# Kernel optimization log

Measured on AMD Instinct MI355X. Metric: run time of the kernel, lower is better.

Reference implementation:

```python
import jax, jax.numpy as jnp
import numpy as np
from jax import lax

D_MODEL = 1024
EXPAND = 2
D_INNER = EXPAND * D_MODEL  # 2048
D_STATE = 16
D_CONV = 4
DT_RANK = -(-D_INNER // 16)  # ceil(d_inner/16) = 128
BATCH, SEQLEN = 2, 1024
LN_EPS = 1e-5


def setup_inputs() -> dict:
    key = jax.random.key(0)
    ks = jax.random.split(key, 8)
    s = lambda n: 1.0 / np.sqrt(n)
    x = jax.random.normal(ks[0], (BATCH, SEQLEN, D_MODEL), jnp.float32)
    ln_gamma = jnp.ones((D_MODEL,), jnp.float32)
    ln_beta = jnp.zeros((D_MODEL,), jnp.float32)
    in_proj_w = jax.random.normal(ks[1], (D_MODEL, 2 * D_INNER), jnp.float32) * s(D_MODEL)
    conv_w = jax.random.normal(ks[2], (D_INNER, D_CONV), jnp.float32) * s(D_CONV)
    conv_b = jnp.zeros((D_INNER,), jnp.float32)
    x_proj_w = jax.random.normal(ks[3], (D_INNER, DT_RANK + 2 * D_STATE), jnp.float32) * s(D_INNER)
    dt_proj_w = jax.random.uniform(ks[4], (DT_RANK, D_INNER), jnp.float32,
                                   -DT_RANK ** -0.5, DT_RANK ** -0.5)
    # dt bias init: inverse-softplus of dt ~ LogUniform(1e-3, 1e-1)
    dt = jnp.exp(jax.random.uniform(ks[5], (D_INNER,), jnp.float32)
                 * (np.log(0.1) - np.log(0.001)) + np.log(0.001))
    dt = jnp.clip(dt, 1e-4)
    dt_proj_b = dt + jnp.log(-jnp.expm1(-dt))
    A_log = jnp.log(jnp.tile(jnp.arange(1, D_STATE + 1, dtype=jnp.float32)[None, :],
                             (D_INNER, 1)))  # (D_INNER, D_STATE)
    D_param = jnp.ones((D_INNER,), jnp.float32)
    out_proj_w = jax.random.normal(ks[6], (D_INNER, D_MODEL), jnp.float32) * s(D_INNER)
    return {"x": x, "ln_gamma": ln_gamma, "ln_beta": ln_beta, "in_proj_w": in_proj_w,
            "conv_w": conv_w, "conv_b": conv_b, "x_proj_w": x_proj_w,
            "dt_proj_w": dt_proj_w, "dt_proj_b": dt_proj_b, "A_log": A_log,
            "D_param": D_param, "out_proj_w": out_proj_w}


def _layernorm(x, gamma, beta):
    mu = jnp.mean(x, -1, keepdims=True)
    var = jnp.mean(jnp.square(x - mu), -1, keepdims=True)
    return (x - mu) * lax.rsqrt(var + LN_EPS) * gamma + beta


def reference(x, ln_gamma, ln_beta, in_proj_w, conv_w, conv_b, x_proj_w,
              dt_proj_w, dt_proj_b, A_log, D_param, out_proj_w):
    B, L, _ = x.shape
    residual = x
    h = _layernorm(x, ln_gamma, ln_beta)
    xz = h @ in_proj_w                               # (B, L, 2*Di)
    xb, z = jnp.split(xz, 2, axis=-1)                # each (B, L, Di)

    # Depthwise causal conv1d (left pad d_conv-1, truncate to L)
    xp = jnp.pad(xb, ((0, 0), (D_CONV - 1, 0), (0, 0)))
    xc = sum(xp[:, k:k + L, :] * conv_w[:, k] for k in range(D_CONV)) + conv_b
    xb = jax.nn.silu(xc)                             # (B, L, Di)

    # Selective SSM
    xpj = xb @ x_proj_w                              # (B, L, dt_rank + 2N)
    dt_r = xpj[..., :DT_RANK]
    B_mat = xpj[..., DT_RANK:DT_RANK + D_STATE]      # (B, L, N)
    C_mat = xpj[..., DT_RANK + D_STATE:]             # (B, L, N)
    delta = jax.nn.softplus(dt_r @ dt_proj_w + dt_proj_b)  # (B, L, Di)
    A = -jnp.exp(A_log)                              # (Di, N)
    dA = jnp.exp(delta[..., None] * A)               # (B, L, Di, N)
    dBx = delta[..., None] * B_mat[:, :, None, :] * xb[..., None]  # (B, L, Di, N)

    def step(hcar, inp):
        dA_t, dBx_t, C_t = inp                       # (B,Di,N),(B,Di,N),(B,N)
        hcar = dA_t * hcar + dBx_t
        y_t = jnp.einsum('bdn,bn->bd', hcar, C_t)
        return hcar, y_t

    h0 = jnp.zeros((B, D_INNER, D_STATE), xb.dtype)
    _, ys = lax.scan(step, h0, (dA.transpose(1, 0, 2, 3),
                                dBx.transpose(1, 0, 2, 3),
                                C_mat.transpose(1, 0, 2)))
    y = ys.transpose(1, 0, 2) + xb * D_param         # (B, L, Di)

    y = y * jax.nn.silu(z)
    return y @ out_proj_w + residual
```

## Files before the change

kernel.cpp:

```cpp
#include <hip/hip_runtime.h>
#include <hip/hip_bf16.h>

#define D_MODEL 1024
#define D_INNER 2048
#define NPROJ   4096
#define D_STATE 16
#define DT_RANK 128
#define XPJ_N   160
#define SEQLEN  1024
#define BATCH   2
#define NTOK    2048
#define CHUNK   32
#define NCHUNK  (SEQLEN / CHUNK)
#define LOG2_NCHUNK 5
#define SPLITK  8
#define OP_SPLITK 4

typedef short short8 __attribute__((ext_vector_type(8)));
typedef float f32x4 __attribute__((ext_vector_type(4)));

__device__ __forceinline__ float sigmoidf_(float x) { return 1.f / (1.f + __expf(-x)); }
__device__ __forceinline__ ushort f2bf_bits(float f) {
    __hip_bfloat16 h = __float2bfloat16(f);
    return *(ushort*)&h;
}
__device__ __forceinline__ float bf2f(ushort u) {
    union { unsigned int i; float f; } v;
    v.i = ((unsigned int)u) << 16;
    return v.f;
}

__global__ __launch_bounds__(256) void ln_kernel(const float* __restrict__ x,
                                                 const float* __restrict__ g,
                                                 const float* __restrict__ be,
                                                 ushort* __restrict__ hb)
{
    int row = blockIdx.x;
    const float4* xr = (const float4*)(x + (long)row * D_MODEL);
    float4 v = xr[threadIdx.x];
    float s1 = v.x + v.y + v.z + v.w;
    float s2 = v.x*v.x + v.y*v.y + v.z*v.z + v.w*v.w;
    for (int off = 32; off >= 1; off >>= 1) {
        s1 += __shfl_down(s1, off);
        s2 += __shfl_down(s2, off);
    }
    __shared__ float red[8];
    int wid = threadIdx.x >> 6;
    if ((threadIdx.x & 63) == 0) { red[wid] = s1; red[4 + wid] = s2; }
    __syncthreads();
    float mu  = (red[0] + red[1] + red[2] + red[3]) * (1.f / D_MODEL);
    float ex2 = (red[4] + red[5] + red[6] + red[7]) * (1.f / D_MODEL);
    float inv = rsqrtf(ex2 - mu * mu + 1e-5f);
    float4 g4 = ((const float4*)g)[threadIdx.x];
    float4 b4 = ((const float4*)be)[threadIdx.x];
    ushort4 o;
    o.x = f2bf_bits((v.x - mu) * inv * g4.x + b4.x);
    o.y = f2bf_bits((v.y - mu) * inv * g4.y + b4.y);
    o.z = f2bf_bits((v.z - mu) * inv * g4.z + b4.z);
    o.w = f2bf_bits((v.w - mu) * inv * g4.w + b4.w);
    *(ushort4*)(hb + (long)row * D_MODEL + threadIdx.x * 4) = o;
}

__global__ __launch_bounds__(256) void transpose_bf16_kernel(const float* __restrict__ in,
                                                             ushort* __restrict__ out,
                                                             int R, int C)
{
    __shared__ float tile[64][65];
    int c0 = blockIdx.x * 64, r0 = blockIdx.y * 64;
    #pragma unroll
    for (int i = 0; i < 16; ++i) {
        int idx = threadIdx.x + i * 256;
        int r = idx >> 6, c = idx & 63;
        tile[r][c] = (r0 + r < R && c0 + c < C) ? in[(long)(r0 + r) * C + (c0 + c)] : 0.f;
    }
    __syncthreads();
    #pragma unroll
    for (int i = 0; i < 16; ++i) {
        int idx = threadIdx.x + i * 256;
        int cc = idx >> 6, rr = idx & 63;
        if (c0 + cc < C && r0 + rr < R)
            out[(long)(c0 + cc) * R + (r0 + rr)] = f2bf_bits(tile[rr][cc]);
    }
}

template <int EPI, int OBF>
__global__ __launch_bounds__(256) void gemm_mfma_kernel(const ushort* __restrict__ A,
                                                        const ushort* __restrict__ Bt,
                                                        const float* __restrict__ bias,
                                                        const float* __restrict__ resid,
                                                        float* __restrict__ Cf,
                                                        ushort* __restrict__ Cb,
                                                        int M, int N, int K, int lda, int ldb)
{
    long zoff = (long)blockIdx.z;
    A  += zoff * K;
    Bt += zoff * K;
    if (OBF == 0) Cf += zoff * (long)M * N;
    __shared__ __align__(16) ushort Al[128 * 32];
    __shared__ __align__(16) ushort Bl[128 * 32];
    int tid = threadIdx.x;
    int lane = tid & 63;
    int w = tid >> 6, wr = w >> 1, wc = w & 1;
    int m0 = blockIdx.y * 128, n0 = blockIdx.x * 128;
    f32x4 acc[4][4];
    #pragma unroll
    for (int m = 0; m < 4; ++m)
        #pragma unroll
        for (int n = 0; n < 4; ++n) acc[m][n] = (f32x4){0.f, 0.f, 0.f, 0.f};
    int l15 = lane & 15, kq = lane >> 4;

    for (int k0 = 0; k0 < K; k0 += 32) {
        #pragma unroll
        for (int i = 0; i < 2; ++i) {
            int s = i * 256 + tid;
            int row = s >> 2, kg = s & 3;
            int kgl = kg ^ ((row >> 1) & 3);
            __builtin_amdgcn_global_load_lds(
                (const __attribute__((address_space(1))) void*)(A + (long)(m0 + row) * lda + k0 + kgl * 8),
                (__attribute__((address_space(3))) void*)(Al + s * 8), 16, 0, 0);
            __builtin_amdgcn_global_load_lds(
                (const __attribute__((address_space(1))) void*)(Bt + (long)(n0 + row) * ldb + k0 + kgl * 8),
                (__attribute__((address_space(3))) void*)(Bl + s * 8), 16, 0, 0);
        }
        __syncthreads();
        short8 af[4], bf[4];
        #pragma unroll
        for (int m = 0; m < 4; ++m) {
            int row = wr * 64 + m * 16 + l15;
            af[m] = *(const short8*)&Al[row * 32 + (kq ^ ((row >> 1) & 3)) * 8];
        }
        #pragma unroll
        for (int n = 0; n < 4; ++n) {
            int row = wc * 64 + n * 16 + l15;
            bf[n] = *(const short8*)&Bl[row * 32 + (kq ^ ((row >> 1) & 3)) * 8];
        }
        #pragma unroll
        for (int m = 0; m < 4; ++m)
            #pragma unroll
            for (int n = 0; n < 4; ++n)
                acc[m][n] = __builtin_amdgcn_mfma_f32_16x16x32_bf16(af[m], bf[n], acc[m][n], 0, 0, 0);
        __syncthreads();
    }
    #pragma unroll
    for (int m = 0; m < 4; ++m) {
        #pragma unroll
        for (int n = 0; n < 4; ++n) {
            #pragma unroll
            for (int r = 0; r < 4; ++r) {
                int row = m0 + wr * 64 + m * 16 + kq * 4 + r;
                int col = n0 + wc * 64 + n * 16 + l15;
                float v = acc[m][n][r];
                if (EPI == 1) {
                    v += bias[col];
                    v = (v > 20.f) ? v : log1pf(__expf(v));
                } else if (EPI == 2) {
                    v += resid[(long)row * N + col];
                }
                if (OBF) Cb[(long)row * N + col] = f2bf_bits(v);
                else     Cf[(long)row * N + col] = v;
            }
        }
    }
}

template <int EPI, int OBF>
__global__ __launch_bounds__(256) void gemm_mfma64_kernel(const ushort* __restrict__ A,
                                                          const ushort* __restrict__ Bt,
                                                          const float* __restrict__ bias,
                                                          const float* __restrict__ resid,
                                                          float* __restrict__ Cf,
                                                          ushort* __restrict__ Cb,
                                                          int M, int N, int K)
{
    __shared__ __align__(16) ushort Al[128 * 32];
    __shared__ __align__(16) ushort Bl[64 * 32];
    int tid = threadIdx.x;
    int lane = tid & 63;
    int w = tid >> 6, wr = w >> 1, wc = w & 1;
    int m0 = blockIdx.y * 128, n0 = blockIdx.x * 64;
    f32x4 acc[4][2];
    #pragma unroll
    for (int m = 0; m < 4; ++m)
        #pragma unroll
        for (int n = 0; n < 2; ++n) acc[m][n] = (f32x4){0.f, 0.f, 0.f, 0.f};
    int l15 = lane & 15, kq = lane >> 4;

    for (int k0 = 0; k0 < K; k0 += 32) {
        #pragma unroll
        for (int i = 0; i < 2; ++i) {
            int s = i * 256 + tid;
            int row = s >> 2, kg = s & 3;
            int kgl = kg ^ ((row >> 1) & 3);
            __builtin_amdgcn_global_load_lds(
                (const __attribute__((address_space(1))) void*)(A + (long)(m0 + row) * K + k0 + kgl * 8),
                (__attribute__((address_space(3))) void*)(Al + s * 8), 16, 0, 0);
        }
        {
            int s = tid;
            int row = s >> 2, kg = s & 3;
            int kgl = kg ^ ((row >> 1) & 3);
            __builtin_amdgcn_global_load_lds(
                (const __attribute__((address_space(1))) void*)(Bt + (long)(n0 + row) * K + k0 + kgl * 8),
                (__attribute__((address_space(3))) void*)(Bl + s * 8), 16, 0, 0);
        }
        __syncthreads();
        short8 af[4], bf[2];
        #pragma unroll
        for (int m = 0; m < 4; ++m) {
            int row = wr * 64 + m * 16 + l15;
            af[m] = *(const short8*)&Al[row * 32 + (kq ^ ((row >> 1) & 3)) * 8];
        }
        #pragma unroll
        for (int n = 0; n < 2; ++n) {
            int row = wc * 32 + n * 16 + l15;
            bf[n] = *(const short8*)&Bl[row * 32 + (kq ^ ((row >> 1) & 3)) * 8];
        }
        #pragma unroll
        for (int m = 0; m < 4; ++m)
            #pragma unroll
            for (int n = 0; n < 2; ++n)
                acc[m][n] = __builtin_amdgcn_mfma_f32_16x16x32_bf16(af[m], bf[n], acc[m][n], 0, 0, 0);
        __syncthreads();
    }
    #pragma unroll
    for (int m = 0; m < 4; ++m) {
        #pragma unroll
        for (int n = 0; n < 2; ++n) {
            #pragma unroll
            for (int r = 0; r < 4; ++r) {
                int row = m0 + wr * 64 + m * 16 + kq * 4 + r;
                int col = n0 + wc * 32 + n * 16 + l15;
                float v = acc[m][n][r];
                if (EPI == 1) {
                    v += bias[col];
                    v = (v > 20.f) ? v : log1pf(__expf(v));
                } else if (EPI == 2) {
                    v += resid[(long)row * N + col];
                }
                if (OBF) Cb[(long)row * N + col] = f2bf_bits(v);
                else     Cf[(long)row * N + col] = v;
            }
        }
    }
}

__global__ __launch_bounds__(256) void reduce_out_kernel(const float* __restrict__ Ppart,
                                                         const float* __restrict__ resid,
                                                         float* __restrict__ out)
{
    long i = (long)blockIdx.x * 256 + threadIdx.x;
    const long STRIDE = (long)NTOK * D_MODEL / 4;
    float4 s = ((const float4*)Ppart)[i];
    #pragma unroll
    for (int k = 1; k < OP_SPLITK; ++k) {
        float4 p = ((const float4*)Ppart)[k * STRIDE + i];
        s.x += p.x; s.y += p.y; s.z += p.z; s.w += p.w;
    }
    float4 r = ((const float4*)resid)[i];
    s.x += r.x; s.y += r.y; s.z += r.z; s.w += r.w;
    ((float4*)out)[i] = s;
}

__global__ __launch_bounds__(256) void gemm4_mfma_kernel(const ushort* __restrict__ A,
                                                         const ushort* __restrict__ Bt,
                                                         float* __restrict__ Ppart,
                                                         int M, int K)
{
    __shared__ __align__(16) ushort Al[64 * 32];
    __shared__ __align__(16) ushort Bl[160 * 32];
    int tid = threadIdx.x;
    int lane = tid & 63;
    int w = tid >> 6, wr = w >> 1, wc = w & 1;
    int sk = blockIdx.x;
    int m0 = blockIdx.y * 64;
    int kbase = sk * (K / SPLITK);
    f32x4 acc[2][5];
    #pragma unroll
    for (int m = 0; m < 2; ++m)
        #pragma unroll
        for (int n = 0; n < 5; ++n) acc[m][n] = (f32x4){0.f, 0.f, 0.f, 0.f};
    int l15 = lane & 15, kq = lane >> 4;

    for (int ks = 0; ks < K / SPLITK; ks += 32) {
        int k0 = kbase + ks;
        {
            int s = tid;
            int row = s >> 2, kg = s & 3;
            int kgl = kg ^ ((row >> 1) & 3);
            __builtin_amdgcn_global_load_lds(
                (const __attribute__((address_space(1))) void*)(A + (long)(m0 + row) * K + k0 + kgl * 8),
                (__attribute__((address_space(3))) void*)(Al + s * 8), 16, 0, 0);
        }
        #pragma unroll
        for (int i = 0; i < 3; ++i) {
            int s = i * 256 + tid;
            if (s < 640) {
                int row = s >> 2, kg = s & 3;
                int kgl = kg ^ ((row >> 1) & 3);
                __builtin_amdgcn_global_load_lds(
                    (const __attribute__((address_space(1))) void*)(Bt + (long)row * K + k0 + kgl * 8),
                    (__attribute__((address_space(3))) void*)(Bl + s * 8), 16, 0, 0);
            }
        }
        __syncthreads();
        short8 af[2], bf[5];
        #pragma unroll
        for (int m = 0; m < 2; ++m) {
            int row = wr * 32 + m * 16 + l15;
            af[m] = *(const short8*)&Al[row * 32 + (kq ^ ((row >> 1) & 3)) * 8];
        }
        #pragma unroll
        for (int n = 0; n < 5; ++n) {
            int row = wc * 80 + n * 16 + l15;
            bf[n] = *(const short8*)&Bl[row * 32 + (kq ^ ((row >> 1) & 3)) * 8];
        }
        #pragma unroll
        for (int m = 0; m < 2; ++m)
            #pragma unroll
            for (int n = 0; n < 5; ++n)
                acc[m][n] = __builtin_amdgcn_mfma_f32_16x16x32_bf16(af[m], bf[n], acc[m][n], 0, 0, 0);
        __syncthreads();
    }
    float* P = Ppart + (long)sk * M * XPJ_N;
    #pragma unroll
    for (int m = 0; m < 2; ++m) {
        #pragma unroll
        for (int n = 0; n < 5; ++n) {
            #pragma unroll
            for (int r = 0; r < 4; ++r) {
                int row = m0 + wr * 32 + m * 16 + kq * 4 + r;
                int col = wc * 80 + n * 16 + l15;
                P[(long)row * XPJ_N + col] = acc[m][n][r];
            }
        }
    }
}

__global__ __launch_bounds__(256) void reduce_xpj_kernel(const float* __restrict__ Ppart,
                                                         float* __restrict__ xpj,
                                                         ushort* __restrict__ dtr)
{
    long i = (long)blockIdx.x * 256 + threadIdx.x;
    float s = 0.f;
    #pragma unroll
    for (int k = 0; k < SPLITK; ++k) s += Ppart[k * (long)NTOK * XPJ_N + i];
    xpj[i] = s;
    int col = (int)(i % XPJ_N);
    long row = i / XPJ_N;
    if (col < DT_RANK) dtr[row * DT_RANK + col] = f2bf_bits(s);
}

__global__ __launch_bounds__(256) void conv_silu_kernel(const ushort* __restrict__ xzb,
                                                        const float* __restrict__ cw,
                                                        const float* __restrict__ cb,
                                                        ushort* __restrict__ xbb)
{
    long i = (long)blockIdx.x * 256 + threadIdx.x;
    int d = (int)(i & (D_INNER - 1));
    long tok = i >> 11;
    int l = (int)(tok & (SEQLEN - 1));
    float w0 = cw[d * 4 + 0], w1 = cw[d * 4 + 1], w2 = cw[d * 4 + 2], w3 = cw[d * 4 + 3];
    float acc = cb[d];
    acc += bf2f(xzb[tok * NPROJ + d]) * w3;
    if (l >= 1) acc += bf2f(xzb[(tok - 1) * NPROJ + d]) * w2;
    if (l >= 2) acc += bf2f(xzb[(tok - 2) * NPROJ + d]) * w1;
    if (l >= 3) acc += bf2f(xzb[(tok - 3) * NPROJ + d]) * w0;
    float v = acc * sigmoidf_(acc);
    xbb[i] = f2bf_bits(v);
}

__global__ __launch_bounds__(256) void scan_partial_kernel(const ushort* __restrict__ deltab,
                                                           const ushort* __restrict__ xbb,
                                                           const float* __restrict__ xpj,
                                                           const float* __restrict__ A_log,
                                                           float* __restrict__ Pout,
                                                           float* __restrict__ Hout)
{
    int tid = threadIdx.x;
    int j = tid & 3, grp = tid >> 2;
    long gidx = (long)blockIdx.x * 64 + grp;
    int d = (int)(gidx & (D_INNER - 1));
    int c = (int)((gidx >> 11) & (NCHUNK - 1));
    int b = (int)(gidx >> (11 + LOG2_NCHUNK));
    float4 al = *(const float4*)&A_log[d * D_STATE + 4 * j];
    float a0 = -__expf(al.x), a1 = -__expf(al.y), a2 = -__expf(al.z), a3 = -__expf(al.w);
    float h0 = 0.f, h1 = 0.f, h2 = 0.f, h3 = 0.f, cum = 0.f;
    long tok0 = (long)b * SEQLEN + c * CHUNK;
    const ushort* dp = deltab + tok0 * D_INNER + d;
    const ushort* xp = xbb + tok0 * D_INNER + d;
    const float* Bp = xpj + tok0 * XPJ_N + DT_RANK + 4 * j;
    for (int t = 0; t < CHUNK; ++t) {
        float dl = bf2f(*dp);
        float x  = bf2f(*xp);
        float4 Bv = *(const float4*)Bp;
        dp += D_INNER; xp += D_INNER; Bp += XPJ_N;
        cum += dl;
        float ux = dl * x;
        h0 = __expf(dl * a0) * h0 + ux * Bv.x;
        h1 = __expf(dl * a1) * h1 + ux * Bv.y;
        h2 = __expf(dl * a2) * h2 + ux * Bv.z;
        h3 = __expf(dl * a3) * h3 + ux * Bv.w;
    }
    long o = gidx * D_STATE + 4 * j;
    *(float4*)&Pout[o] = (float4){__expf(a0 * cum), __expf(a1 * cum), __expf(a2 * cum), __expf(a3 * cum)};
    *(float4*)&Hout[o] = (float4){h0, h1, h2, h3};
}

__global__ __launch_bounds__(256) void scan_chunkscan_kernel(const float* __restrict__ P,
                                                             const float* __restrict__ H,
                                                             float* __restrict__ hinit)
{
    long i = (long)blockIdx.x * 256 + threadIdx.x;
    int n = (int)(i & (D_STATE - 1));
    int d = (int)((i >> 4) & (D_INNER - 1));
    int b = (int)(i >> 15);
    float h = 0.f;
    for (int c = 0; c < NCHUNK; ++c) {
        long o = ((((long)b * NCHUNK + c) * D_INNER + d) * D_STATE) + n;
        hinit[o] = h;
        h = P[o] * h + H[o];
    }
}

__global__ __launch_bounds__(256) void scan_final_kernel(const ushort* __restrict__ deltab,
                                                         const ushort* __restrict__ xbb,
                                                         const float* __restrict__ xpj,
                                                         const ushort* __restrict__ xzb,
                                                         const float* __restrict__ A_log,
                                                         const float* __restrict__ Dp,
                                                         const float* __restrict__ hinit,
                                                         ushort* __restrict__ yb)
{
    int tid = threadIdx.x;
    int j = tid & 3, grp = tid >> 2;
    long gidx = (long)blockIdx.x * 64 + grp;
    int d = (int)(gidx & (D_INNER - 1));
    int c = (int)((gidx >> 11) & (NCHUNK - 1));
    int b = (int)(gidx >> (11 + LOG2_NCHUNK));
    float4 al = *(const float4*)&A_log[d * D_STATE + 4 * j];
    float a0 = -__expf(al.x), a1 = -__expf(al.y), a2 = -__expf(al.z), a3 = -__expf(al.w);
    float dpar = Dp[d];
    float4 hv = *(const float4*)&hinit[gidx * D_STATE + 4 * j];
    float h0 = hv.x, h1 = hv.y, h2 = hv.z, h3 = hv.w;
    long tok0 = (long)b * SEQLEN + c * CHUNK;
    const ushort* dp = deltab + tok0 * D_INNER + d;
    const ushort* xp = xbb + tok0 * D_INNER + d;
    const float* Bp = xpj + tok0 * XPJ_N + DT_RANK + 4 * j;
    const float* Cp = Bp + D_STATE;
    const ushort* zp = xzb + tok0 * NPROJ + D_INNER + d;
    ushort* yp = yb + tok0 * D_INNER + d;
    for (int t = 0; t < CHUNK; ++t) {
        float dl = bf2f(*dp);
        float x  = bf2f(*xp);
        float4 Bv = *(const float4*)Bp;
        float4 Cv = *(const float4*)Cp;
        dp += D_INNER; xp += D_INNER; Bp += XPJ_N; Cp += XPJ_N;
        float ux = dl * x;
        h0 = __expf(dl * a0) * h0 + ux * Bv.x;
        h1 = __expf(dl * a1) * h1 + ux * Bv.y;
        h2 = __expf(dl * a2) * h2 + ux * Bv.z;
        h3 = __expf(dl * a3) * h3 + ux * Bv.w;
        float p = h0 * Cv.x + h1 * Cv.y + h2 * Cv.z + h3 * Cv.w;
        p += __shfl_xor(p, 1);
        p += __shfl_xor(p, 2);
        if (j == 0) {
            float z = bf2f(*zp);
            float y = p + x * dpar;
            *yp = f2bf_bits(y * (z * sigmoidf_(z)));
        }
        zp += NPROJ; yp += D_INNER;
    }
}

extern "C" void kernel_launch(void* const* d_in, const int* in_sizes, int n_in,
                              void* d_out, int out_size, void* d_ws, size_t ws_size,
                              hipStream_t stream) {
    const float* x         = (const float*)d_in[0];
    const float* ln_gamma  = (const float*)d_in[1];
    const float* ln_beta   = (const float*)d_in[2];
    const float* in_proj_w = (const float*)d_in[3];
    const float* conv_w    = (const float*)d_in[4];
    const float* conv_b    = (const float*)d_in[5];
    const float* x_proj_w  = (const float*)d_in[6];
    const float* dt_proj_w = (const float*)d_in[7];
    const float* dt_proj_b = (const float*)d_in[8];
    const float* A_log     = (const float*)d_in[9];
    const float* D_param   = (const float*)d_in[10];
    const float* out_proj_w= (const float*)d_in[11];
    float* out = (float*)d_out;

    float* ws = (float*)d_ws;
    float* h     = ws;
    float* xz    = h     + (long)NTOK * D_MODEL;
    float* xb    = xz    + (long)NTOK * NPROJ;
    float* xpj   = xb    + (long)NTOK * D_INNER;
    float* delta = xpj   + (long)NTOK * XPJ_N;
    float* yfin  = delta + (long)NTOK * D_INNER;

    const long PH = (long)BATCH * NCHUNK * D_INNER * D_STATE;
    ushort* h_bf16   = (ushort*)h;
    ushort* DTT      = (ushort*)(h + 1048576);
    float*  hinit    = h;
    ushort* xz_bf16  = (ushort*)xz;
    ushort* W7T      = (ushort*)(xz + 4194304);
    ushort* W2T      = (ushort*)xb;
    ushort* xb_bf16  = (ushort*)xb;
    ushort* XPT      = (ushort*)xpj;
    ushort* delta_bf16 = (ushort*)delta;
    float*  Ppart    = yfin;
    ushort* dtr      = (ushort*)(yfin + (long)SPLITK * NTOK * XPJ_N);
    float*  Pbuf     = yfin;
    float*  Hbuf     = yfin + PH;
    ushort* y_bf16   = (ushort*)yfin;
    float*  PpartO   = xb;

    transpose_bf16_kernel<<<dim3(NPROJ / 64, D_MODEL / 64), 256, 0, stream>>>(
        in_proj_w, W2T, D_MODEL, NPROJ);
    transpose_bf16_kernel<<<dim3(D_MODEL / 64, D_INNER / 64), 256, 0, stream>>>(
        out_proj_w, W7T, D_INNER, D_MODEL);

    ln_kernel<<<NTOK, 256, 0, stream>>>(x, ln_gamma, ln_beta, h_bf16);

    gemm_mfma_kernel<0, 1><<<dim3(NPROJ / 128, NTOK / 128), 256, 0, stream>>>(
        h_bf16, W2T, nullptr, nullptr, nullptr, xz_bf16,
        NTOK, NPROJ, D_MODEL, D_MODEL, D_MODEL);

    conv_silu_kernel<<<(NTOK * D_INNER) / 256, 256, 0, stream>>>(
        xz_bf16, conv_w, conv_b, xb_bf16);

    transpose_bf16_kernel<<<dim3((XPJ_N + 63) / 64, D_INNER / 64), 256, 0, stream>>>(
        x_proj_w, XPT, D_INNER, XPJ_N);
    transpose_bf16_kernel<<<dim3(D_INNER / 64, DT_RANK / 64), 256, 0, stream>>>(
        dt_proj_w, DTT, DT_RANK, D_INNER);

    gemm4_mfma_kernel<<<dim3(SPLITK, NTOK / 64), 256, 0, stream>>>(
        xb_bf16, XPT, Ppart, NTOK, D_INNER);
    reduce_xpj_kernel<<<(NTOK * XPJ_N) / 256, 256, 0, stream>>>(Ppart, xpj, dtr);

    gemm_mfma64_kernel<1, 1><<<dim3(D_INNER / 64, NTOK / 128), 256, 0, stream>>>(
        dtr, DTT, dt_proj_b, nullptr, nullptr, delta_bf16, NTOK, D_INNER, DT_RANK);

    scan_partial_kernel<<<(BATCH * NCHUNK * D_INNER) / 64, 256, 0, stream>>>(
        delta_bf16, xb_bf16, xpj, A_log, Pbuf, Hbuf);
    scan_chunkscan_kernel<<<(BATCH * D_INNER * D_STATE) / 256, 256, 0, stream>>>(
        Pbuf, Hbuf, hinit);
    scan_final_kernel<<<(BATCH * NCHUNK * D_INNER) / 64, 256, 0, stream>>>(
        delta_bf16, xb_bf16, xpj, xz_bf16, A_log, D_param, hinit, y_bf16);

    gemm_mfma_kernel<0, 0><<<dim3(D_MODEL / 128, NTOK / 128, OP_SPLITK), 256, 0, stream>>>(
        y_bf16, W7T, nullptr, nullptr, PpartO, nullptr, NTOK, D_MODEL, D_INNER / OP_SPLITK,
        D_INNER, D_INNER);
    reduce_out_kernel<<<(NTOK * D_MODEL / 4) / 256, 256, 0, stream>>>(PpartO, x, out);
}
```

Before: 203.9 us.

## Store scan inputs channel-major so scan kernels read contiguous vectors

The in_proj GEMM epilogue now writes x to a compact buffer and z transposed (channel-major), and the dt_proj GEMM writes delta transposed. A new bf16 transpose kernel produces a channel-major copy of xb. The scan kernels read 8 timesteps per vector load instead of strided scalar loads, and use exp2f with pre-scaled A. The scan output is produced channel-major and transposed back before the out_proj GEMM. This replaces strided per-timestep global accesses in the scans, at the cost of two extra transpose launches and a larger workspace layout.

```diff
diff --git a/kernel.cpp b/kernel.cpp
--- a/kernel.cpp
+++ b/kernel.cpp
@@ -12,11 +12,12 @@
 #define NTOK    2048
 #define CHUNK   32
 #define NCHUNK  (SEQLEN / CHUNK)
-#define LOG2_NCHUNK 5
 #define SPLITK  8
 #define OP_SPLITK 4
 
 typedef short short8 __attribute__((ext_vector_type(8)));
+typedef unsigned short ushort8v __attribute__((ext_vector_type(8)));
+typedef unsigned short ushort4v __attribute__((ext_vector_type(4)));
 typedef float f32x4 __attribute__((ext_vector_type(4)));
 
 __device__ __forceinline__ float sigmoidf_(float x) { return 1.f / (1.f + __expf(-x)); }
@@ -29,6 +30,7 @@
     v.i = ((unsigned int)u) << 16;
     return v.f;
 }
+#define LOG2E 1.44269504088896f
 
 __global__ __launch_bounds__(256) void ln_kernel(const float* __restrict__ x,
                                                  const float* __restrict__ g,
@@ -83,19 +85,46 @@
     }
 }
 
-template <int EPI, int OBF>
+__global__ __launch_bounds__(256) void transpose_bb_kernel(const ushort* __restrict__ in,
+                                                           ushort* __restrict__ out,
+                                                           int R, int C)
+{
+    __shared__ ushort tile[64][68];
+    int c0 = blockIdx.x * 64, r0 = blockIdx.y * 64;
+    #pragma unroll
+    for (int i = 0; i < 4; ++i) {
+        int idx = threadIdx.x + i * 256;
+        int r = idx >> 4, cq = idx & 15;
+        ushort4v v = *(const ushort4v*)(in + (long)(r0 + r) * C + c0 + cq * 4);
+        *(ushort4v*)&tile[r][cq * 4] = v;
+    }
+    __syncthreads();
+    #pragma unroll
+    for (int i = 0; i < 4; ++i) {
+        int idx = threadIdx.x + i * 256;
+        int cc = idx >> 4, rq = idx & 15;
+        ushort4v v;
+        v.x = tile[rq * 4 + 0][cc];
+        v.y = tile[rq * 4 + 1][cc];
+        v.z = tile[rq * 4 + 2][cc];
+        v.w = tile[rq * 4 + 3][cc];
+        *(ushort4v*)(out + (long)(c0 + cc) * R + r0 + rq * 4) = v;
+    }
+}
+
+template <int EPI, int OMODE>
 __global__ __launch_bounds__(256) void gemm_mfma_kernel(const ushort* __restrict__ A,
                                                         const ushort* __restrict__ Bt,
                                                         const float* __restrict__ bias,
-                                                        const float* __restrict__ resid,
                                                         float* __restrict__ Cf,
                                                         ushort* __restrict__ Cb,
+                                                        ushort* __restrict__ Cb2,
                                                         int M, int N, int K, int lda, int ldb)
 {
     long zoff = (long)blockIdx.z;
     A  += zoff * K;
     Bt += zoff * K;
-    if (OBF == 0) Cf += zoff * (long)M * N;
+    if (OMODE == 0) Cf += zoff * (long)M * N;
     __shared__ __align__(16) ushort Al[128 * 32];
     __shared__ __align__(16) ushort Bl[128 * 32];
     int tid = threadIdx.x;
@@ -145,32 +174,43 @@
     for (int m = 0; m < 4; ++m) {
         #pragma unroll
         for (int n = 0; n < 4; ++n) {
+            int rowb = m0 + wr * 64 + m * 16 + kq * 4;
+            int col  = n0 + wc * 64 + n * 16 + l15;
+            float v0[4];
             #pragma unroll
             for (int r = 0; r < 4; ++r) {
-                int row = m0 + wr * 64 + m * 16 + kq * 4 + r;
-                int col = n0 + wc * 64 + n * 16 + l15;
                 float v = acc[m][n][r];
                 if (EPI == 1) {
                     v += bias[col];
                     v = (v > 20.f) ? v : log1pf(__expf(v));
-                } else if (EPI == 2) {
-                    v += resid[(long)row * N + col];
                 }
-                if (OBF) Cb[(long)row * N + col] = f2bf_bits(v);
-                else     Cf[(long)row * N + col] = v;
+                v0[r] = v;
             }
-        }
-    }
-}
-
-template <int EPI, int OBF>
-__global__ __launch_bounds__(256) void gemm_mfma64_kernel(const ushort* __restrict__ A,
-                                                          const ushort* __restrict__ Bt,
-                                                          const float* __restrict__ bias,
-                                                          const float* __restrict__ resid,
-                                                          float* __restrict__ Cf,
-                                                          ushort* __restrict__ Cb,
-                                                          int M, int N, int K)
+            if (OMODE == 0) {
+                #pragma unroll
+                for (int r = 0; r < 4; ++r)
+                    Cf[(long)(rowb + r) * N + col] = v0[r];
+            } else {
+                if (col < D_INNER) {
+                    #pragma unroll
+                    for (int r = 0; r < 4; ++r)
+                        Cb[(long)(rowb + r) * D_INNER + col] = f2bf_bits(v0[r]);
+                } else {
+                    ushort4v pk;
+                    pk.x = f2bf_bits(v0[0]); pk.y = f2bf_bits(v0[1]);
+                    pk.z = f2bf_bits(v0[2]); pk.w = f2bf_bits(v0[3]);
+                    *(ushort4v*)(Cb2 + (long)(col - D_INNER) * M + rowb) = pk;
+                }
+            }
+        }
+    }
+}
+
+__global__ __launch_bounds__(256) void gemm_mfma64T_kernel(const ushort* __restrict__ A,
+                                                           const ushort* __restrict__ Bt,
+                                                           const float* __restrict__ bias,
+                                                           ushort* __restrict__ CbT,
+                                                           int M, int N, int K)
 {
     __shared__ __align__(16) ushort Al[128 * 32];
     __shared__ __align__(16) ushort Bl[64 * 32];
@@ -226,20 +266,16 @@
     for (int m = 0; m < 4; ++m) {
         #pragma unroll
         for (int n = 0; n < 2; ++n) {
+            int rowb = m0 + wr * 64 + m * 16 + kq * 4;
+            int col  = n0 + wc * 32 + n * 16 + l15;
+            ushort4v pk;
             #pragma unroll
             for (int r = 0; r < 4; ++r) {
-                int row = m0 + wr * 64 + m * 16 + kq * 4 + r;
-                int col = n0 + wc * 32 + n * 16 + l15;
-                float v = acc[m][n][r];
-                if (EPI == 1) {
-                    v += bias[col];
-                    v = (v > 20.f) ? v : log1pf(__expf(v));
-                } else if (EPI == 2) {
-                    v += resid[(long)row * N + col];
-                }
-                if (OBF) Cb[(long)row * N + col] = f2bf_bits(v);
-                else     Cf[(long)row * N + col] = v;
+                float v = acc[m][n][r] + bias[col];
+                v = (v > 20.f) ? v : log1pf(__expf(v));
+                ((ushort*)&pk)[r] = f2bf_bits(v);
             }
+            *(ushort4v*)(CbT + (long)col * M + rowb) = pk;
         }
     }
 }
@@ -361,16 +397,16 @@
     int l = (int)(tok & (SEQLEN - 1));
     float w0 = cw[d * 4 + 0], w1 = cw[d * 4 + 1], w2 = cw[d * 4 + 2], w3 = cw[d * 4 + 3];
     float acc = cb[d];
-    acc += bf2f(xzb[tok * NPROJ + d]) * w3;
-    if (l >= 1) acc += bf2f(xzb[(tok - 1) * NPROJ + d]) * w2;
-    if (l >= 2) acc += bf2f(xzb[(tok - 2) * NPROJ + d]) * w1;
-    if (l >= 3) acc += bf2f(xzb[(tok - 3) * NPROJ + d]) * w0;
+    acc += bf2f(xzb[tok * D_INNER + d]) * w3;
+    if (l >= 1) acc += bf2f(xzb[(tok - 1) * D_INNER + d]) * w2;
+    if (l >= 2) acc += bf2f(xzb[(tok - 2) * D_INNER + d]) * w1;
+    if (l >= 3) acc += bf2f(xzb[(tok - 3) * D_INNER + d]) * w0;
     float v = acc * sigmoidf_(acc);
     xbb[i] = f2bf_bits(v);
 }
 
-__global__ __launch_bounds__(256) void scan_partial_kernel(const ushort* __restrict__ deltab,
-                                                           const ushort* __restrict__ xbb,
+__global__ __launch_bounds__(256) void scan_partial_kernel(const ushort* __restrict__ deltaT,
+                                                           const ushort* __restrict__ xbT,
                                                            const float* __restrict__ xpj,
                                                            const float* __restrict__ A_log,
                                                            float* __restrict__ Pout,
@@ -381,28 +417,34 @@
     long gidx = (long)blockIdx.x * 64 + grp;
     int d = (int)(gidx & (D_INNER - 1));
     int c = (int)((gidx >> 11) & (NCHUNK - 1));
-    int b = (int)(gidx >> (11 + LOG2_NCHUNK));
+    int b = (int)(gidx >> 16);
     float4 al = *(const float4*)&A_log[d * D_STATE + 4 * j];
-    float a0 = -__expf(al.x), a1 = -__expf(al.y), a2 = -__expf(al.z), a3 = -__expf(al.w);
+    float a0 = -__expf(al.x) * LOG2E, a1 = -__expf(al.y) * LOG2E;
+    float a2 = -__expf(al.z) * LOG2E, a3 = -__expf(al.w) * LOG2E;
     float h0 = 0.f, h1 = 0.f, h2 = 0.f, h3 = 0.f, cum = 0.f;
     long tok0 = (long)b * SEQLEN + c * CHUNK;
-    const ushort* dp = deltab + tok0 * D_INNER + d;
-    const ushort* xp = xbb + tok0 * D_INNER + d;
+    const ushort* dp = deltaT + (long)d * NTOK + tok0;
+    const ushort* xp = xbT + (long)d * NTOK + tok0;
     const float* Bp = xpj + tok0 * XPJ_N + DT_RANK + 4 * j;
-    for (int t = 0; t < CHUNK; ++t) {
-        float dl = bf2f(*dp);
-        float x  = bf2f(*xp);
-        float4 Bv = *(const float4*)Bp;
-        dp += D_INNER; xp += D_INNER; Bp += XPJ_N;
-        cum += dl;
-        float ux = dl * x;
-        h0 = __expf(dl * a0) * h0 + ux * Bv.x;
-        h1 = __expf(dl * a1) * h1 + ux * Bv.y;
-        h2 = __expf(dl * a2) * h2 + ux * Bv.z;
-        h3 = __expf(dl * a3) * h3 + ux * Bv.w;
+    #pragma unroll
+    for (int t8 = 0; t8 < CHUNK / 8; ++t8) {
+        ushort8v dl8 = *(const ushort8v*)dp; dp += 8;
+        ushort8v x8  = *(const ushort8v*)xp; xp += 8;
+        #pragma unroll
+        for (int k = 0; k < 8; ++k) {
+            float dl = bf2f(dl8[k]);
+            float x  = bf2f(x8[k]);
+            float4 Bv = *(const float4*)Bp; Bp += XPJ_N;
+            cum += dl;
+            float ux = dl * x;
+            h0 = exp2f(dl * a0) * h0 + ux * Bv.x;
+            h1 = exp2f(dl * a1) * h1 + ux * Bv.y;
+            h2 = exp2f(dl * a2) * h2 + ux * Bv.z;
+            h3 = exp2f(dl * a3) * h3 + ux * Bv.w;
+        }
     }
     long o = gidx * D_STATE + 4 * j;
-    *(float4*)&Pout[o] = (float4){__expf(a0 * cum), __expf(a1 * cum), __expf(a2 * cum), __expf(a3 * cum)};
+    *(float4*)&Pout[o] = (float4){exp2f(a0 * cum), exp2f(a1 * cum), exp2f(a2 * cum), exp2f(a3 * cum)};
     *(float4*)&Hout[o] = (float4){h0, h1, h2, h3};
 }
 
@@ -422,53 +464,63 @@
     }
 }
 
-__global__ __launch_bounds__(256) void scan_final_kernel(const ushort* __restrict__ deltab,
-                                                         const ushort* __restrict__ xbb,
+__global__ __launch_bounds__(256) void scan_final_kernel(const ushort* __restrict__ deltaT,
+                                                         const ushort* __restrict__ xbT,
                                                          const float* __restrict__ xpj,
-                                                         const ushort* __restrict__ xzb,
+                                                         const ushort* __restrict__ zT,
                                                          const float* __restrict__ A_log,
                                                          const float* __restrict__ Dp,
                                                          const float* __restrict__ hinit,
-                                                         ushort* __restrict__ yb)
+                                                         ushort* __restrict__ yT)
 {
     int tid = threadIdx.x;
     int j = tid & 3, grp = tid >> 2;
     long gidx = (long)blockIdx.x * 64 + grp;
     int d = (int)(gidx & (D_INNER - 1));
     int c = (int)((gidx >> 11) & (NCHUNK - 1));
-    int b = (int)(gidx >> (11 + LOG2_NCHUNK));
+    int b = (int)(gidx >> 16);
     float4 al = *(const float4*)&A_log[d * D_STATE + 4 * j];
-    float a0 = -__expf(al.x), a1 = -__expf(al.y), a2 = -__expf(al.z), a3 = -__expf(al.w);
+    float a0 = -__expf(al.x) * LOG2E, a1 = -__expf(al.y) * LOG2E;
+    float a2 = -__expf(al.z) * LOG2E, a3 = -__expf(al.w) * LOG2E;
     float dpar = Dp[d];
     float4 hv = *(const float4*)&hinit[gidx * D_STATE + 4 * j];
     float h0 = hv.x, h1 = hv.y, h2 = hv.z, h3 = hv.w;
     long tok0 = (long)b * SEQLEN + c * CHUNK;
-    const ushort* dp = deltab + tok0 * D_INNER + d;
-    const ushort* xp = xbb + tok0 * D_INNER + d;
+    const ushort* dp = deltaT + (long)d * NTOK + tok0;
+    const ushort* xp = xbT + (long)d * NTOK + tok0;
+    const ushort* zp = zT + (long)d * NTOK + tok0;
+    ushort* yp = yT + (long)d * NTOK + tok0;
     const float* Bp = xpj + tok0 * XPJ_N + DT_RANK + 4 * j;
-    const float* Cp = Bp + D_STATE;
-    const ushort* zp = xzb + tok0 * NPROJ + D_INNER + d;
-    ushort* yp = yb + tok0 * D_INNER + d;
-    for (int t = 0; t < CHUNK; ++t) {
-        float dl = bf2f(*dp);
-        float x  = bf2f(*xp);
-        float4 Bv = *(const float4*)Bp;
-        float4 Cv = *(const float4*)Cp;
-        dp += D_INNER; xp += D_INNER; Bp += XPJ_N; Cp += XPJ_N;
-        float ux = dl * x;
-        h0 = __expf(dl * a0) * h0 + ux * Bv.x;
-        h1 = __expf(dl * a1) * h1 + ux * Bv.y;
-        h2 = __expf(dl * a2) * h2 + ux * Bv.z;
-        h3 = __expf(dl * a3) * h3 + ux * Bv.w;
-        float p = h0 * Cv.x + h1 * Cv.y + h2 * Cv.z + h3 * Cv.w;
-        p += __shfl_xor(p, 1);
-        p += __shfl_xor(p, 2);
-        if (j == 0) {
-            float z = bf2f(*zp);
-            float y = p + x * dpar;
-            *yp = f2bf_bits(y * (z * sigmoidf_(z)));
-        }
-        zp += NPROJ; yp += D_INNER;
+    #pragma unroll
+    for (int t8 = 0; t8 < CHUNK / 8; ++t8) {
+        ushort8v dl8 = *(const ushort8v*)dp; dp += 8;
+        ushort8v x8  = *(const ushort8v*)xp; xp += 8;
+        ushort8v z8 = {0,0,0,0,0,0,0,0};
+        if (j == 0) z8 = *(const ushort8v*)zp;
+        zp += 8;
+        ushort8v y8;
+        #pragma unroll
+        for (int k = 0; k < 8; ++k) {
+            float dl = bf2f(dl8[k]);
+            float x  = bf2f(x8[k]);
+            float4 Bv = *(const float4*)Bp;
+            float4 Cv = *(const float4*)(Bp + D_STATE);
+            Bp += XPJ_N;
+            float ux = dl * x;
+            h0 = exp2f(dl * a0) * h0 + ux * Bv.x;
+            h1 = exp2f(dl * a1) * h1 + ux * Bv.y;
+            h2 = exp2f(dl * a2) * h2 + ux * Bv.z;
+            h3 = exp2f(dl * a3) * h3 + ux * Bv.w;
+            float p = h0 * Cv.x + h1 * Cv.y + h2 * Cv.z + h3 * Cv.w;
+            p += __shfl_xor(p, 1);
+            p += __shfl_xor(p, 2);
+            if (j == 0) {
+                float z = bf2f(z8[k]);
+                y8[k] = f2bf_bits((p + x * dpar) * (z * sigmoidf_(z)));
+            }
+        }
+        if (j == 0) *(ushort8v*)yp = y8;
+        yp += 8;
     }
 }
 
@@ -489,66 +541,66 @@
     const float* out_proj_w= (const float*)d_in[11];
     float* out = (float*)d_out;
 
-    float* ws = (float*)d_ws;
-    float* h     = ws;
-    float* xz    = h     + (long)NTOK * D_MODEL;
-    float* xb    = xz    + (long)NTOK * NPROJ;
-    float* xpj   = xb    + (long)NTOK * D_INNER;
-    float* delta = xpj   + (long)NTOK * XPJ_N;
-    float* yfin  = delta + (long)NTOK * D_INNER;
-
-    const long PH = (long)BATCH * NCHUNK * D_INNER * D_STATE;
-    ushort* h_bf16   = (ushort*)h;
-    ushort* DTT      = (ushort*)(h + 1048576);
-    float*  hinit    = h;
-    ushort* xz_bf16  = (ushort*)xz;
-    ushort* W7T      = (ushort*)(xz + 4194304);
-    ushort* W2T      = (ushort*)xb;
-    ushort* xb_bf16  = (ushort*)xb;
-    ushort* XPT      = (ushort*)xpj;
-    ushort* delta_bf16 = (ushort*)delta;
-    float*  Ppart    = yfin;
-    ushort* dtr      = (ushort*)(yfin + (long)SPLITK * NTOK * XPJ_N);
-    float*  Pbuf     = yfin;
-    float*  Hbuf     = yfin + PH;
-    ushort* y_bf16   = (ushort*)yfin;
-    float*  PpartO   = xb;
+    float* p = (float*)d_ws;
+    ushort* hb     = (ushort*)p; p += 1048576;
+    ushort* W2T    = (ushort*)p; p += 2097152;
+    ushort* W7T    = (ushort*)p; p += 1048576;
+    ushort* XPT    = (ushort*)p; p += 163840;
+    ushort* DTT    = (ushort*)p; p += 131072;
+    ushort* xzb    = (ushort*)p; p += 2097152;
+    ushort* zT     = (ushort*)p; p += 2097152;
+    ushort* xbb    = (ushort*)p; p += 2097152;
+    ushort* xbT    = (ushort*)p; p += 2097152;
+    float*  xpj    = p;          p += 327680;
+    ushort* dtr    = (ushort*)p; p += 131072;
+    ushort* deltaT = (ushort*)p; p += 2097152;
+    float*  Ppart  = p;          p += 2621440;
+    float*  Pbuf   = p;          p += 2097152;
+    float*  Hbuf   = p;          p += 2097152;
+    float*  hinit  = p;          p += 2097152;
+    ushort* yT     = (ushort*)p; p += 2097152;
+    ushort* yb     = (ushort*)p; p += 2097152;
+    float*  PpartO = p;          p += 8388608;
 
     transpose_bf16_kernel<<<dim3(NPROJ / 64, D_MODEL / 64), 256, 0, stream>>>(
         in_proj_w, W2T, D_MODEL, NPROJ);
     transpose_bf16_kernel<<<dim3(D_MODEL / 64, D_INNER / 64), 256, 0, stream>>>(
         out_proj_w, W7T, D_INNER, D_MODEL);
-
-    ln_kernel<<<NTOK, 256, 0, stream>>>(x, ln_gamma, ln_beta, h_bf16);
-
-    gemm_mfma_kernel<0, 1><<<dim3(NPROJ / 128, NTOK / 128), 256, 0, stream>>>(
-        h_bf16, W2T, nullptr, nullptr, nullptr, xz_bf16,
-        NTOK, NPROJ, D_MODEL, D_MODEL, D_MODEL);
-
-    conv_silu_kernel<<<(NTOK * D_INNER) / 256, 256, 0, stream>>>(
-        xz_bf16, conv_w, conv_b, xb_bf16);
-
     transpose_bf16_kernel<<<dim3((XPJ_N + 63) / 64, D_INNER / 64), 256, 0, stream>>>(
         x_proj_w, XPT, D_INNER, XPJ_N);
     transpose_bf16_kernel<<<dim3(D_INNER / 64, DT_RANK / 64), 256, 0, stream>>>(
         dt_proj_w, DTT, DT_RANK, D_INNER);
 
+    ln_kernel<<<NTOK, 256, 0, stream>>>(x, ln_gamma, ln_beta, hb);
+
+    gemm_mfma_kernel<0, 2><<<dim3(NPROJ / 128, NTOK / 128), 256, 0, stream>>>(
+        hb, W2T, nullptr, nullptr, xzb, zT, NTOK, NPROJ, D_MODEL, D_MODEL, D_MODEL);
+
+    conv_silu_kernel<<<(NTOK * D_INNER) / 256, 256, 0, stream>>>(
+        xzb, conv_w, conv_b, xbb);
+
+    transpose_bb_kernel<<<dim3(D_INNER / 64, NTOK / 64), 256, 0, stream>>>(
+        xbb, xbT, NTOK, D_INNER);
+
     gemm4_mfma_kernel<<<dim3(SPLITK, NTOK / 64), 256, 0, stream>>>(
-        xb_bf16, XPT, Ppart, NTOK, D_INNER);
+        xbb, XPT, Ppart, NTOK, D_INNER);
     reduce_xpj_kernel<<<(NTOK * XPJ_N) / 256, 256, 0, stream>>>(Ppart, xpj, dtr);
 
-    gemm_mfma64_kernel<1, 1><<<dim3(D_INNER / 64, NTOK / 128), 256, 0, stream>>>(
-        dtr, DTT, dt_proj_b, nullptr, nullptr, delta_bf16, NTOK, D_INNER, DT_RANK);
+    gemm_mfma64T_kernel<<<dim3(D_INNER / 64, NTOK / 128), 256, 0, stream>>>(
+        dtr, DTT, dt_proj_b, deltaT, NTOK, D_INNER, DT_RANK);
 
     scan_partial_kernel<<<(BATCH * NCHUNK * D_INNER) / 64, 256, 0, stream>>>(
-        delta_bf16, xb_bf16, xpj, A_log, Pbuf, Hbuf);
+        deltaT, xbT, xpj, A_log, Pbuf, Hbuf);
     scan_chunkscan_kernel<<<(BATCH * D_INNER * D_STATE) / 256, 256, 0, stream>>>(
         Pbuf, Hbuf, hinit);
     scan_final_kernel<<<(BATCH * NCHUNK * D_INNER) / 64, 256, 0, stream>>>(
-        delta_bf16, xb_bf16, xpj, xz_bf16, A_log, D_param, hinit, y_bf16);
+        deltaT, xbT, xpj, zT, A_log, D_param, hinit, yT);
+
+    transpose_bb_kernel<<<dim3(NTOK / 64, D_INNER / 64), 256, 0, stream>>>(
+        yT, yb, D_INNER, NTOK);
 
     gemm_mfma_kernel<0, 0><<<dim3(D_MODEL / 128, NTOK / 128, OP_SPLITK), 256, 0, stream>>>(
-        y_bf16, W7T, nullptr, nullptr, PpartO, nullptr, NTOK, D_MODEL, D_INNER / OP_SPLITK,
+        yb, W7T, nullptr, PpartO, nullptr, nullptr, NTOK, D_MODEL, D_INNER / OP_SPLITK,
         D_INNER, D_INNER);
     reduce_out_kernel<<<(NTOK * D_MODEL / 4) / 256, 256, 0, stream>>>(PpartO, x, out);
 }
```

Result: slower. 218.3 us (+7.1%).
